# Kernel tuning notes

Measured on AMD Instinct MI355X. Metric: run time of the kernel, lower is better.

The kernel has to match this reference:

```python
import jax, jax.numpy as jnp
import numpy as np

# dims
N, T = 16, 2000            # batch, encoder frames
ENC, DEC = 512, 512        # enc_dim, dec_dim
ATT, C, K, H = 512, 10, 64, 4  # att_dim, conv_channels, loc_context, att_head


def setup_inputs() -> dict:
    key = jax.random.key(0)
    ks = jax.random.split(key, 16)
    s = 0.02
    enc_pad = jax.random.normal(ks[0], (N, T, ENC), jnp.float32)
    enc_len = jax.random.randint(ks[1], (N,), T // 2, T + 1, jnp.int32)
    dec_prev = jax.random.normal(ks[2], (N, DEC), jnp.float32)
    ali_prev = jax.random.uniform(ks[3], (N, H, T), jnp.float32)
    ali_prev = ali_prev / ali_prev.sum(-1, keepdims=True)
    # parameters (torch layout)
    We = jax.random.normal(ks[4], (ATT * H, ENC), jnp.float32) * s   # enc_proj weight
    be = jnp.zeros((ATT * H,), jnp.float32)                          # enc_proj bias
    Wk = jax.random.normal(ks[5], (ATT * H, ENC), jnp.float32) * s   # key_proj
    Wd = jax.random.normal(ks[6], (ATT * H, DEC), jnp.float32) * s   # dec_proj
    WF = jax.random.normal(ks[7], (C * H, 1, 2 * K + 1), jnp.float32) * s  # F: grouped conv1d
    bF = jnp.zeros((C * H,), jnp.float32)
    Wa = jax.random.normal(ks[8], (H, ATT, C), jnp.float32) * s      # att: 1x1 grouped conv, per-head [ATT,C]
    Ww = jax.random.normal(ks[9], (H, ATT), jnp.float32) * s         # w: 1x1 grouped conv, per-head [ATT]
    Wc = jax.random.normal(ks[10], (ENC, ATT * H), jnp.float32) * s  # ctx_proj
    bc = jnp.zeros((ENC,), jnp.float32)
    return {"enc_pad": enc_pad, "enc_len": enc_len, "dec_prev": dec_prev,
            "ali_prev": ali_prev, "We": We, "be": be, "Wk": Wk, "Wd": Wd,
            "WF": WF, "bF": bF, "Wa": Wa, "Ww": Ww, "Wc": Wc, "bc": bc}


def reference(enc_pad, enc_len, dec_prev, ali_prev, We, be, Wk, Wd, WF, bF, Wa, Ww, Wc, bc):
    n, t, _ = enc_pad.shape
    # enc_part: N x H x T x D
    ep = enc_pad @ We.T + be
    enc_part = ep.reshape(n, t, H, ATT).transpose(0, 2, 1, 3)
    # key_part: N x H x D x T (matches torch transpose(1,2).view ordering)
    kp = enc_pad @ Wk.T
    key_part = kp.transpose(0, 2, 1).reshape(n, H, ATT, t)
    # pad mask: N x T, True where padded
    pad_mask = jnp.arange(t)[None, :] >= enc_len[:, None]
    # location features: grouped conv1d over alignment, per head
    f = jax.lax.conv_general_dilated(
        ali_prev, WF, window_strides=(1,), padding=[(K, K)],
        dimension_numbers=("NCH", "OIH", "NCH"), feature_group_count=H)
    f = (f + bF[None, :, None]).reshape(n, H, C, t)
    # 1x1 grouped conv: C -> ATT per head
    att_part = jnp.einsum("hdc,nhct->nhdt", Wa, f)
    dec_part = (dec_prev @ Wd.T).reshape(n, H, ATT)
    sum_part = jnp.tanh(att_part + key_part + dec_part[..., None])  # N x H x D x T
    score = jnp.einsum("hd,nhdt->nht", Ww, sum_part)                # N x H x T
    score = jnp.where(pad_mask[:, None, :], -jnp.inf, score)
    ali = jax.nn.softmax(score, axis=-1)
    ctx = jnp.einsum("nht,nhtd->nhd", ali, enc_part).reshape(n, H * ATT)
    ctx = ctx @ Wc.T + bc
    return ali, ctx
```

## Files before the change

kernel.cpp:

```cpp
#include <hip/hip_runtime.h>

#define NB   16
#define TT   2000
#define TP   2048
#define ENC  512
#define ATTD 512
#define HH   4
#define CC   10
#define KK   64
#define KW   129
#define HATT 2048

typedef unsigned short u16;
typedef __attribute__((ext_vector_type(8))) short bf16x8;
typedef __attribute__((ext_vector_type(4))) float f32x4;

#define AS1 __attribute__((address_space(1)))
#define AS3 __attribute__((address_space(3)))

__device__ inline unsigned bfpack2(float lo, float hi) {
    unsigned a = __builtin_bit_cast(unsigned, lo);
    unsigned b = __builtin_bit_cast(unsigned, hi);
    a = (a + 0x7fffu + ((a >> 16) & 1u)) >> 16;
    b = (b + 0x7fffu + ((b >> 16) & 1u)) >> 16;
    return a | (b << 16);
}

__global__ __launch_bounds__(256) void prep_kernel(
    const float* __restrict__ enc, const float* __restrict__ Wk,
    const float* __restrict__ ali_prev, const float* __restrict__ WF,
    const float* __restrict__ bF, const float* __restrict__ dec_prev,
    const float* __restrict__ Wd, const float* __restrict__ Wa,
    u16* __restrict__ Abf, u16* __restrict__ Wkbf,
    u16* __restrict__ ftb, u16* __restrict__ wab,
    float* __restrict__ decp)
{
    __shared__ union {
        struct { float aliW[632]; float wfT[KW * CC]; float bfs[CC]; } cv;
        float dsl[16 * 128];
    } sm;
    const int bid = blockIdx.x, tid = threadIdx.x;

    if (bid < 8704) {
        long long gid = ((long long)bid * 256 + tid) * 8;
        const long long ATOT = (long long)NB * TP * ENC;
        if (gid < ATOT) {
            int n = (int)(gid >> 20);
            int rem = (int)(gid & ((1 << 20) - 1));
            int r = rem >> 9, e = rem & 511;
            uint4 out;
            if (r < TT) {
                const float* s = enc + ((long long)n * TT + r) * ENC + e;
                float4 v0 = *(const float4*)s;
                float4 v1 = *(const float4*)(s + 4);
                out.x = bfpack2(v0.x, v0.y); out.y = bfpack2(v0.z, v0.w);
                out.z = bfpack2(v1.x, v1.y); out.w = bfpack2(v1.z, v1.w);
            } else {
                out.x = out.y = out.z = out.w = 0u;
            }
            *(uint4*)(Abf + gid) = out;
        } else {
            long long j = gid - ATOT;
            const float* s = Wk + j;
            float4 v0 = *(const float4*)s;
            float4 v1 = *(const float4*)(s + 4);
            uint4 out;
            out.x = bfpack2(v0.x, v0.y); out.y = bfpack2(v0.z, v0.w);
            out.z = bfpack2(v1.x, v1.y); out.w = bfpack2(v1.z, v1.w);
            *(uint4*)(Wkbf + j) = out;
        }
    } else if (bid < 8960) {
        int b2 = bid - 8704;
        int tc = b2 & 3, h = (b2 >> 2) & 3, n = b2 >> 4;
        int t0 = tc * 500;
        float* aliW = sm.cv.aliW;
        float* wfT  = sm.cv.wfT;
        float* bfs  = sm.cv.bfs;
        const float* arow = ali_prev + ((long long)n * HH + h) * TT;
        for (int i = tid; i < 632; i += 256) {
            int tt = t0 - KK + i;
            aliW[i] = (tt >= 0 && tt < TT) ? arow[tt] : 0.f;
        }
        for (int i = tid; i < KW * CC; i += 256) {
            int k = i / CC, c = i - k * CC;
            wfT[i] = WF[(h * CC + c) * KW + k];
        }
        if (tid < CC) bfs[tid] = bF[h * CC + tid];
        __syncthreads();
        if (tid < 250) {
            float acc0[CC], acc1[CC];
            #pragma unroll
            for (int c = 0; c < CC; c++) { acc0[c] = 0.f; acc1[c] = 0.f; }
            const int base = 2 * tid;
            float2 w0 = *(const float2*)&aliW[base];
            for (int k = 0; k < 128; k += 2) {
                float2 w2 = *(const float2*)&aliW[base + k + 2];
                #pragma unroll
                for (int cj = 0; cj < 5; cj++) {
                    float2 fk  = *(const float2*)&wfT[k * CC + cj * 2];
                    float2 fk1 = *(const float2*)&wfT[(k + 1) * CC + cj * 2];
                    acc0[2*cj]   += w0.x * fk.x + w0.y * fk1.x;
                    acc0[2*cj+1] += w0.x * fk.y + w0.y * fk1.y;
                    acc1[2*cj]   += w0.y * fk.x + w2.x * fk1.x;
                    acc1[2*cj+1] += w0.y * fk.y + w2.x * fk1.y;
                }
                w0 = w2;
            }
            #pragma unroll
            for (int cj = 0; cj < 5; cj++) {
                float2 fk = *(const float2*)&wfT[128 * CC + cj * 2];
                acc0[2*cj]   += w0.x * fk.x;  acc0[2*cj+1] += w0.x * fk.y;
                acc1[2*cj]   += w0.y * fk.x;  acc1[2*cj+1] += w0.y * fk.y;
            }
            #pragma unroll
            for (int c = 0; c < CC; c++) { acc0[c] += bfs[c]; acc1[c] += bfs[c]; }
            int t = t0 + base;
            u16* frow = ftb + (((long long)(n * HH + h)) * TP + t) * 16;
            uint4 ra, rb;
            ra.x = bfpack2(acc0[0], acc0[1]); ra.y = bfpack2(acc0[2], acc0[3]);
            ra.z = bfpack2(acc0[4], acc0[5]); ra.w = bfpack2(acc0[6], acc0[7]);
            rb.x = bfpack2(acc0[8], acc0[9]); rb.y = 0u; rb.z = 0u; rb.w = 0u;
            *(uint4*)(frow)     = ra; *(uint4*)(frow + 8)  = rb;
            ra.x = bfpack2(acc1[0], acc1[1]); ra.y = bfpack2(acc1[2], acc1[3]);
            ra.z = bfpack2(acc1[4], acc1[5]); ra.w = bfpack2(acc1[6], acc1[7]);
            rb.x = bfpack2(acc1[8], acc1[9]);
            *(uint4*)(frow + 16) = ra; *(uint4*)(frow + 24) = rb;
        } else if (tc == 3) {
            uint4 z = {0u, 0u, 0u, 0u};
            int r0 = 2000 + (tid - 250) * 8;
            u16* frow = ftb + (((long long)(n * HH + h)) * TP + r0) * 16;
            for (int r = 0; r < 8; r++) {
                *(uint4*)(frow + r * 16)     = z;
                *(uint4*)(frow + r * 16 + 8) = z;
            }
        }
    } else if (bid < 8992) {
        int b2 = bid - 8960;
        int kc = b2 >> 3, jc = b2 & 7;
        for (int i = tid; i < 2048; i += 256) {
            int nn = i >> 7, kk = i & 127;
            sm.dsl[i] = dec_prev[nn * 512 + kc * 128 + kk];
        }
        __syncthreads();
        int d = jc * 256 + tid;
        float acc[NB];
        #pragma unroll
        for (int n = 0; n < NB; n++) acc[n] = 0.f;
        const float4* w4 = (const float4*)(Wd + (long long)d * 512 + kc * 128);
        for (int e4 = 0; e4 < 32; e4++) {
            float4 w = w4[e4];
            #pragma unroll
            for (int n = 0; n < NB; n++) {
                const float* a = sm.dsl + n * 128 + e4 * 4;
                acc[n] += w.x * a[0] + w.y * a[1] + w.z * a[2] + w.w * a[3];
            }
        }
        #pragma unroll
        for (int n = 0; n < NB; n++) decp[((long long)kc * NB + n) * HATT + d] = acc[n];
    } else {
        int b2 = bid - 8992;
        int j0 = b2 * 512 + tid * 2;
        #pragma unroll
        for (int q = 0; q < 2; q++) {
            int j = j0 + q;
            int hh = j >> 9, dd = j & 511;
            const float* wr = Wa + ((long long)(hh * ATTD + dd)) * CC;
            uint4 ra, rb;
            ra.x = bfpack2(wr[0], wr[1]); ra.y = bfpack2(wr[2], wr[3]);
            ra.z = bfpack2(wr[4], wr[5]); ra.w = bfpack2(wr[6], wr[7]);
            rb.x = bfpack2(wr[8], wr[9]); rb.y = 0u; rb.z = 0u; rb.w = 0u;
            u16* out = wab + (long long)j * 16;
            *(uint4*)(out)     = ra;
            *(uint4*)(out + 8) = rb;
        }
    }
}

__global__ __launch_bounds__(256, 4) void score_gemm_kernel(
    const u16* __restrict__ Abf, const u16* __restrict__ Bbf,
    const u16* __restrict__ ftb, const u16* __restrict__ wab,
    const float* __restrict__ decp, const float* __restrict__ Ww,
    const int* __restrict__ enc_len, float* __restrict__ score_part)
{
    __shared__ __attribute__((aligned(16))) char smem[40960];
    float* sred = (float*)smem;

    const int bid = blockIdx.x;
    const int swz = (bid & 7) * 512 + (bid >> 3);
    const int nt = swz & 15, mt = (swz >> 4) & 15, n = swz >> 8;

    if (mt * 128 >= enc_len[n]) return;

    const int tid = threadIdx.x, wave = tid >> 6, lane = tid & 63;
    const int l16 = lane & 15, lk = lane >> 4;
    const int h = nt >> 2;

    const u16* Aptr = Abf + ((long long)n * TP + mt * 128) * ENC;
    const u16* Bptr = Bbf + (long long)nt * 128 * ENC;

    f32x4 acc[4][4];
    #pragma unroll
    for (int mi = 0; mi < 4; mi++)
        #pragma unroll
        for (int nj = 0; nj < 4; nj++) {
            f32x4 z = {0.f, 0.f, 0.f, 0.f};
            acc[mi][nj] = z;
        }

    const int wrow = (wave >> 1) * 64, wcol = (wave & 1) * 64;
    const int t0 = mt * 128, dd0 = (nt & 3) * 128;

    {
        const char* eAsrc = (const char*)(ftb + (((long long)(n * HH + h)) * TP + t0) * 16);
        const char* eBsrc = (const char*)(wab + (long long)nt * 128 * 16);
        __builtin_amdgcn_global_load_lds(
            (const AS1 void*)(eAsrc + tid * 16),
            (AS3 void*)(smem + 32768 + wave * 1024), 16, 0, 0);
        __builtin_amdgcn_global_load_lds(
            (const AS1 void*)(eBsrc + tid * 16),
            (AS3 void*)(smem + 36864 + wave * 1024), 16, 0, 0);
    }

    for (int kt = 0; kt < 8; kt++) {
        const int k0 = kt * 64;
        #pragma unroll
        for (int i = 0; i < 4; i++) {
            int b = i * 4096 + tid * 16;
            int r = b >> 7, kb = b & 127;
            int kbs = kb ^ ((r & 7) << 4);
            __builtin_amdgcn_global_load_lds(
                (const AS1 void*)(Aptr + r * ENC + k0 + (kbs >> 1)),
                (AS3 void*)(smem + i * 4096 + wave * 1024), 16, 0, 0);
            __builtin_amdgcn_global_load_lds(
                (const AS1 void*)(Bptr + r * ENC + k0 + (kbs >> 1)),
                (AS3 void*)(smem + 16384 + i * 4096 + wave * 1024), 16, 0, 0);
        }
        __syncthreads();
        #pragma unroll
        for (int ks = 0; ks < 64; ks += 32) {
            bf16x8 af[4], bf[4];
            #pragma unroll
            for (int mi = 0; mi < 4; mi++) {
                int row = wrow + mi * 16 + l16;
                int cb = (ks * 2 + lk * 16) ^ ((row & 7) << 4);
                af[mi] = *(const bf16x8*)(smem + row * 128 + cb);
            }
            #pragma unroll
            for (int nj = 0; nj < 4; nj++) {
                int row = wcol + nj * 16 + l16;
                int cb = (ks * 2 + lk * 16) ^ ((row & 7) << 4);
                bf[nj] = *(const bf16x8*)(smem + 16384 + row * 128 + cb);
            }
            #pragma unroll
            for (int mi = 0; mi < 4; mi++)
                #pragma unroll
                for (int nj = 0; nj < 4; nj++)
                    acc[mi][nj] = __builtin_amdgcn_mfma_f32_16x16x32_bf16(
                        af[mi], bf[nj], acc[mi][nj], 0, 0, 0);
        }
        __syncthreads();
    }

    {
        const u16* eA = (const u16*)(smem + 32768);
        const u16* eB = (const u16*)(smem + 36864);
        bf16x8 zer = {0, 0, 0, 0, 0, 0, 0, 0};
        bf16x8 af[4], bf[4];
        #pragma unroll
        for (int mi = 0; mi < 4; mi++) {
            af[mi] = zer;
            if (lk < 2) af[mi] = *(const bf16x8*)(eA + (wrow + mi * 16 + l16) * 16 + lk * 8);
        }
        #pragma unroll
        for (int nj = 0; nj < 4; nj++) {
            bf[nj] = zer;
            if (lk < 2) bf[nj] = *(const bf16x8*)(eB + (wcol + nj * 16 + l16) * 16 + lk * 8);
        }
        #pragma unroll
        for (int mi = 0; mi < 4; mi++)
            #pragma unroll
            for (int nj = 0; nj < 4; nj++)
                acc[mi][nj] = __builtin_amdgcn_mfma_f32_16x16x32_bf16(
                    af[mi], bf[nj], acc[mi][nj], 0, 0, 0);
    }

    float wm2[4], dec4[4];
    #pragma unroll
    for (int nj = 0; nj < 4; nj++) {
        int cl = wcol + nj * 16 + l16;
        wm2[nj] = -2.f * Ww[h * ATTD + dd0 + cl];
        int j = nt * 128 + cl;
        dec4[nj] = decp[((long long)0 * NB + n) * HATT + j]
                 + decp[((long long)1 * NB + n) * HATT + j]
                 + decp[((long long)2 * NB + n) * HATT + j]
                 + decp[((long long)3 * NB + n) * HATT + j];
    }

    #pragma unroll
    for (int mi = 0; mi < 4; mi++) {
        #pragma unroll
        for (int j = 0; j < 4; j++) {
            int rl = wrow + mi * 16 + lk * 4 + j;
            float s = 0.f;
            #pragma unroll
            for (int nj = 0; nj < 4; nj++) {
                float v = acc[mi][nj][j] + dec4[nj];
                float e = __expf(v + v);
                s = fmaf(wm2[nj], __builtin_amdgcn_rcpf(e + 1.f), s);
            }
            s += __shfl_xor(s, 1); s += __shfl_xor(s, 2);
            s += __shfl_xor(s, 4); s += __shfl_xor(s, 8);
            if (l16 == 0) sred[(wave & 1) * 128 + rl] = s;
        }
    }
    __syncthreads();
    if (tid < 128) {
        int t = t0 + tid;
        if (t < TT)
            score_part[((long long)((nt & 3) * NB + n) * HH + h) * TT + t] =
                sred[tid] + sred[128 + tid];
    }
}

__global__ __launch_bounds__(256) void softmax_kernel(
    const float* __restrict__ score_part, const int* __restrict__ enc_len,
    float* __restrict__ ali)
{
    int n = blockIdx.x >> 2, h = blockIdx.x & 3;
    int len = enc_len[n];
    int tid = threadIdx.x;
    float s[8];
    float lmax = -3.4e38f;
    #pragma unroll
    for (int i = 0; i < 8; i++) {
        int t = tid + i * 256;
        float v = -3.4e38f;
        if (t < len) {
            v = 0.f;
            #pragma unroll
            for (int q = 0; q < 4; q++)
                v += score_part[((long long)(q * NB + n) * HH + h) * TT + t];
        }
        s[i] = v;
        lmax = fmaxf(lmax, v);
    }
    __shared__ float red[256];
    red[tid] = lmax; __syncthreads();
    for (int off = 128; off; off >>= 1) {
        if (tid < off) red[tid] = fmaxf(red[tid], red[tid + off]);
        __syncthreads();
    }
    float bmax = red[0];
    __syncthreads();
    float lsum = 0.f;
    #pragma unroll
    for (int i = 0; i < 8; i++) {
        int t = tid + i * 256;
        if (t < len) { s[i] = expf(s[i] - bmax); lsum += s[i]; }
        else s[i] = 0.f;
    }
    red[tid] = lsum; __syncthreads();
    for (int off = 128; off; off >>= 1) {
        if (tid < off) red[tid] += red[tid + off];
        __syncthreads();
    }
    float inv = 1.f / red[0];
    float* arow = ali + ((long long)n * HH + h) * TT;
    #pragma unroll
    for (int i = 0; i < 8; i++) {
        int t = tid + i * 256;
        if (t < TT) arow[t] = s[i] * inv;
    }
}

__global__ __launch_bounds__(256) void a_enc_kernel(
    const float* __restrict__ ali, const u16* __restrict__ Abf,
    const int* __restrict__ enc_len, float* __restrict__ a_enc_part)
{
    int tc = blockIdx.x & 31, n = blockIdx.x >> 5;
    int tid = threadIdx.x;
    int len = enc_len[n];
    int tbeg = tc * 63;
    int cnt = len - tbeg; if (cnt > 63) cnt = 63; if (cnt < 0) cnt = 0;
    __shared__ float aliS[HH][64];
    {
        int hh = tid >> 6, tt = tid & 63;
        aliS[hh][tt] = (tt < cnt) ? ali[((long long)n * HH + hh) * TT + tbeg + tt] : 0.f;
    }
    __syncthreads();
    float acc[HH][2];
    #pragma unroll
    for (int hh = 0; hh < HH; hh++) { acc[hh][0] = 0.f; acc[hh][1] = 0.f; }
    #pragma unroll 4
    for (int tt = 0; tt < cnt; tt++) {
        int t = tbeg + tt;
        float w0 = aliS[0][tt], w1 = aliS[1][tt], w2 = aliS[2][tt], w3 = aliS[3][tt];
        unsigned u = *(const unsigned*)(Abf + ((long long)n * TP + t) * ENC + tid * 2);
        float ex = __builtin_bit_cast(float, u << 16);
        float ey = __builtin_bit_cast(float, u & 0xffff0000u);
        acc[0][0] += w0 * ex; acc[0][1] += w0 * ey;
        acc[1][0] += w1 * ex; acc[1][1] += w1 * ey;
        acc[2][0] += w2 * ex; acc[2][1] += w2 * ey;
        acc[3][0] += w3 * ex; acc[3][1] += w3 * ey;
    }
    #pragma unroll
    for (int hh = 0; hh < HH; hh++) {
        a_enc_part[(((long long)tc * NB + n) * HH + hh) * ENC + tid * 2 + 0] = acc[hh][0];
        a_enc_part[(((long long)tc * NB + n) * HH + hh) * ENC + tid * 2 + 1] = acc[hh][1];
    }
}

__global__ __launch_bounds__(256) void ctx_tmp_kernel(
    const float* __restrict__ a_enc_part, const float* __restrict__ We,
    const float* __restrict__ be, float* __restrict__ ctmp)
{
    int kc = blockIdx.x >> 3, jc = blockIdx.x & 7;
    int tid = threadIdx.x;
    int j = jc * 256 + tid;
    int h = j >> 9;
    __shared__ float aes[16 * 128];
    for (int i = tid; i < 2048; i += 256) {
        int nn = i >> 7, kk = i & 127;
        float s = 0.f;
        for (int tc = 0; tc < 32; tc++)
            s += a_enc_part[(((long long)tc * NB + nn) * HH + h) * ENC + kc * 128 + kk];
        aes[i] = s;
    }
    __syncthreads();
    float acc[NB];
    #pragma unroll
    for (int n = 0; n < NB; n++) acc[n] = 0.f;
    const float4* w4 = (const float4*)(We + (long long)j * 512 + kc * 128);
    for (int e4 = 0; e4 < 32; e4++) {
        float4 w = w4[e4];
        #pragma unroll
        for (int n = 0; n < NB; n++) {
            const float* a = aes + n * 128 + e4 * 4;
            acc[n] += w.x * a[0] + w.y * a[1] + w.z * a[2] + w.w * a[3];
        }
    }
    float bias = (kc == 0) ? be[j] : 0.f;
    #pragma unroll
    for (int n = 0; n < NB; n++)
        ctmp[((long long)kc * NB + n) * HATT + j] = acc[n] + bias;
}

__global__ __launch_bounds__(256) void ctx_out_kernel(
    const float* __restrict__ ctmp, const float* __restrict__ Wc,
    const float* __restrict__ bc, float* __restrict__ out_ctx)
{
    int ec = blockIdx.x & 7, nc = blockIdx.x >> 3;
    int tid = threadIdx.x;
    __shared__ float ct[8 * 2048];
    __shared__ float red[4][64][8];
    for (int i = tid; i < 8 * 2048; i += 256) {
        int nn = i >> 11, j = i & 2047;
        int n = nc * 8 + nn;
        ct[i] = ctmp[((long long)0 * NB + n) * HATT + j]
              + ctmp[((long long)1 * NB + n) * HATT + j]
              + ctmp[((long long)2 * NB + n) * HATT + j]
              + ctmp[((long long)3 * NB + n) * HATT + j];
    }
    __syncthreads();
    int eo = tid & 63, kq = tid >> 6;
    int eg = ec * 64 + eo;
    float acc[8];
    #pragma unroll
    for (int nn = 0; nn < 8; nn++) acc[nn] = 0.f;
    const float4* w4 = (const float4*)(Wc + (long long)eg * HATT + kq * 512);
    for (int j4 = 0; j4 < 128; j4++) {
        float4 w = w4[j4];
        #pragma unroll
        for (int nn = 0; nn < 8; nn++) {
            const float* a = ct + nn * 2048 + kq * 512 + j4 * 4;
            acc[nn] += w.x * a[0] + w.y * a[1] + w.z * a[2] + w.w * a[3];
        }
    }
    #pragma unroll
    for (int nn = 0; nn < 8; nn++) red[kq][eo][nn] = acc[nn];
    __syncthreads();
    #pragma unroll
    for (int r = 0; r < 2; r++) {
        int idx = tid + r * 256;
        int eo2 = idx & 63, nn2 = idx >> 6;
        float s = red[0][eo2][nn2] + red[1][eo2][nn2]
                + red[2][eo2][nn2] + red[3][eo2][nn2];
        out_ctx[((long long)(nc * 8 + nn2)) * 512 + ec * 64 + eo2] = s + bc[ec * 64 + eo2];
    }
}

extern "C" void kernel_launch(void* const* d_in, const int* in_sizes, int n_in,
                              void* d_out, int out_size, void* d_ws, size_t ws_size,
                              hipStream_t stream)
{
    (void)in_sizes; (void)n_in; (void)out_size; (void)ws_size;
    const float* enc_pad  = (const float*)d_in[0];
    const int*   enc_len  = (const int*)  d_in[1];
    const float* dec_prev = (const float*)d_in[2];
    const float* ali_prev = (const float*)d_in[3];
    const float* We = (const float*)d_in[4];
    const float* be = (const float*)d_in[5];
    const float* Wk = (const float*)d_in[6];
    const float* Wd = (const float*)d_in[7];
    const float* WF = (const float*)d_in[8];
    const float* bF = (const float*)d_in[9];
    const float* Wa = (const float*)d_in[10];
    const float* Ww = (const float*)d_in[11];
    const float* Wc = (const float*)d_in[12];
    const float* bc = (const float*)d_in[13];

    char* ws = (char*)d_ws;
    u16*   Abf  = (u16*)  (ws);
    u16*   Wkbf = (u16*)  (ws + 33554432);
    u16*   ftb  = (u16*)  (ws + 35651584);
    u16*   wab  = (u16*)  (ws + 39845888);
    float* decp = (float*)(ws + 39911424);
    float* spart= (float*)(ws + 40435712);
    float* aep  = (float*)(ws + 40435712);
    float* ctmp = (float*)(ws + 39911424);

    float* ali = (float*)d_out;
    float* ctx = (float*)d_out + NB * HH * TT;

    prep_kernel      <<<8996, 256, 0, stream>>>(enc_pad, Wk, ali_prev, WF, bF,
                                                dec_prev, Wd, Wa,
                                                Abf, Wkbf, ftb, wab, decp);
    score_gemm_kernel<<<4096, 256, 0, stream>>>(Abf, Wkbf, ftb, wab, decp, Ww,
                                                enc_len, spart);
    softmax_kernel   <<<64,   256, 0, stream>>>(spart, enc_len, ali);
    a_enc_kernel     <<<512,  256, 0, stream>>>(ali, Abf, enc_len, aep);
    ctx_tmp_kernel   <<<32,   256, 0, stream>>>(aep, We, be, ctmp);
    ctx_out_kernel   <<<16,   256, 0, stream>>>(ctmp, Wc, bc, ctx);
}
```

Measured before the change: 191.8 us.

## Skip padded rows, vectorise softmax/a_enc, and widen ctx kernels' grids

The prep kernel now converts only encoder rows below each sequence's length and no longer writes zeros for padded rows. Score partials use a padded 2048 stride so the softmax can read and write them with float4. The a_enc kernel splits time across two thread halves, loads 4 bf16 per lane and reduces through shared memory. ctx_tmp and ctx_out double their block counts by halving their K/E chunks, and ctmp moves in the workspace to hold 8 partial slices. Skipping padded rows leaves stale data in Abf, so correctness depends on every consumer masking by enc_len; the score GEMM reads those rows too.

Measured after the change: 182.6 us. 1.05x faster.

```diff
diff --git a/kernel.cpp b/kernel.cpp
--- a/kernel.cpp
+++ b/kernel.cpp
@@ -3,6 +3,7 @@
 #define NB   16
 #define TT   2000
 #define TP   2048
+#define SPT  2048
 #define ENC  512
 #define ATTD 512
 #define HH   4
@@ -31,6 +32,7 @@
     const float* __restrict__ ali_prev, const float* __restrict__ WF,
     const float* __restrict__ bF, const float* __restrict__ dec_prev,
     const float* __restrict__ Wd, const float* __restrict__ Wa,
+    const int* __restrict__ enc_len,
     u16* __restrict__ Abf, u16* __restrict__ Wkbf,
     u16* __restrict__ ftb, u16* __restrict__ wab,
     float* __restrict__ decp)
@@ -48,17 +50,15 @@
             int n = (int)(gid >> 20);
             int rem = (int)(gid & ((1 << 20) - 1));
             int r = rem >> 9, e = rem & 511;
-            uint4 out;
-            if (r < TT) {
+            if (r < enc_len[n]) {
                 const float* s = enc + ((long long)n * TT + r) * ENC + e;
                 float4 v0 = *(const float4*)s;
                 float4 v1 = *(const float4*)(s + 4);
+                uint4 out;
                 out.x = bfpack2(v0.x, v0.y); out.y = bfpack2(v0.z, v0.w);
                 out.z = bfpack2(v1.x, v1.y); out.w = bfpack2(v1.z, v1.w);
-            } else {
-                out.x = out.y = out.z = out.w = 0u;
-            }
-            *(uint4*)(Abf + gid) = out;
+                *(uint4*)(Abf + gid) = out;
+            }
         } else {
             long long j = gid - ATOT;
             const float* s = Wk + j;
@@ -317,7 +317,7 @@
     if (tid < 128) {
         int t = t0 + tid;
         if (t < TT)
-            score_part[((long long)((nt & 3) * NB + n) * HH + h) * TT + t] =
+            score_part[((long long)((nt & 3) * NB + n) * HH + h) * SPT + t] =
                 sred[tid] + sred[128 + tid];
     }
 }
@@ -329,20 +329,22 @@
     int n = blockIdx.x >> 2, h = blockIdx.x & 3;
     int len = enc_len[n];
     int tid = threadIdx.x;
+    int t0 = tid * 8;
     float s[8];
+    #pragma unroll
+    for (int i = 0; i < 8; i++) s[i] = 0.f;
+    #pragma unroll
+    for (int q = 0; q < 4; q++) {
+        const float* rb = score_part + (((long long)(q * NB + n)) * HH + h) * SPT + t0;
+        float4 a = *(const float4*)rb;
+        float4 b = *(const float4*)(rb + 4);
+        s[0] += a.x; s[1] += a.y; s[2] += a.z; s[3] += a.w;
+        s[4] += b.x; s[5] += b.y; s[6] += b.z; s[7] += b.w;
+    }
     float lmax = -3.4e38f;
     #pragma unroll
     for (int i = 0; i < 8; i++) {
-        int t = tid + i * 256;
-        float v = -3.4e38f;
-        if (t < len) {
-            v = 0.f;
-            #pragma unroll
-            for (int q = 0; q < 4; q++)
-                v += score_part[((long long)(q * NB + n) * HH + h) * TT + t];
-        }
-        s[i] = v;
-        lmax = fmaxf(lmax, v);
+        if (t0 + i < len) lmax = fmaxf(lmax, s[i]);
     }
     __shared__ float red[256];
     red[tid] = lmax; __syncthreads();
@@ -355,8 +357,7 @@
     float lsum = 0.f;
     #pragma unroll
     for (int i = 0; i < 8; i++) {
-        int t = tid + i * 256;
-        if (t < len) { s[i] = expf(s[i] - bmax); lsum += s[i]; }
+        if (t0 + i < len) { s[i] = expf(s[i] - bmax); lsum += s[i]; }
         else s[i] = 0.f;
     }
     red[tid] = lsum; __syncthreads();
@@ -366,16 +367,20 @@
     }
     float inv = 1.f / red[0];
     float* arow = ali + ((long long)n * HH + h) * TT;
-    #pragma unroll
-    for (int i = 0; i < 8; i++) {
-        int t = tid + i * 256;
-        if (t < TT) arow[t] = s[i] * inv;
+    if (t0 + 8 <= TT) {
+        float4 o0 = {s[0] * inv, s[1] * inv, s[2] * inv, s[3] * inv};
+        float4 o1 = {s[4] * inv, s[5] * inv, s[6] * inv, s[7] * inv};
+        *(float4*)(arow + t0) = o0;
+        *(float4*)(arow + t0 + 4) = o1;
+    } else {
+        for (int i = 0; i < 8; i++)
+            if (t0 + i < TT) arow[t0 + i] = s[i] * inv;
     }
 }
 
 __global__ __launch_bounds__(256) void a_enc_kernel(
     const float* __restrict__ ali, const u16* __restrict__ Abf,
-    const int* __restrict__ enc_len, float* __restrict__ a_enc_part)
+    const int* __restrict__ enc_len, float* __restrict__ aep)
 {
     int tc = blockIdx.x & 31, n = blockIdx.x >> 5;
     int tid = threadIdx.x;
@@ -383,59 +388,75 @@
     int tbeg = tc * 63;
     int cnt = len - tbeg; if (cnt > 63) cnt = 63; if (cnt < 0) cnt = 0;
     __shared__ float aliS[HH][64];
+    __shared__ float red[2][4][129];
     {
         int hh = tid >> 6, tt = tid & 63;
         aliS[hh][tt] = (tt < cnt) ? ali[((long long)n * HH + hh) * TT + tbeg + tt] : 0.f;
     }
     __syncthreads();
-    float acc[HH][2];
-    #pragma unroll
-    for (int hh = 0; hh < HH; hh++) { acc[hh][0] = 0.f; acc[hh][1] = 0.f; }
-    #pragma unroll 4
-    for (int tt = 0; tt < cnt; tt++) {
-        int t = tbeg + tt;
-        float w0 = aliS[0][tt], w1 = aliS[1][tt], w2 = aliS[2][tt], w3 = aliS[3][tt];
-        unsigned u = *(const unsigned*)(Abf + ((long long)n * TP + t) * ENC + tid * 2);
-        float ex = __builtin_bit_cast(float, u << 16);
-        float ey = __builtin_bit_cast(float, u & 0xffff0000u);
-        acc[0][0] += w0 * ex; acc[0][1] += w0 * ey;
-        acc[1][0] += w1 * ex; acc[1][1] += w1 * ey;
-        acc[2][0] += w2 * ex; acc[2][1] += w2 * ey;
-        acc[3][0] += w3 * ex; acc[3][1] += w3 * ey;
+    const int l = tid & 127, tq = tid >> 7;
+    float acc[HH][4];
+    #pragma unroll
+    for (int hh = 0; hh < HH; hh++)
+        #pragma unroll
+        for (int k = 0; k < 4; k++) acc[hh][k] = 0.f;
+    for (int ii = 0; ii < 32; ii++) {
+        int tl = ii * 2 + tq;
+        if (tl < cnt) {
+            uint2 u = *(const uint2*)(Abf + ((long long)n * TP + tbeg + tl) * ENC + l * 4);
+            float e0 = __builtin_bit_cast(float, u.x << 16);
+            float e1 = __builtin_bit_cast(float, u.x & 0xffff0000u);
+            float e2 = __builtin_bit_cast(float, u.y << 16);
+            float e3 = __builtin_bit_cast(float, u.y & 0xffff0000u);
+            #pragma unroll
+            for (int hh = 0; hh < HH; hh++) {
+                float w = aliS[hh][tl];
+                acc[hh][0] += w * e0; acc[hh][1] += w * e1;
+                acc[hh][2] += w * e2; acc[hh][3] += w * e3;
+            }
+        }
     }
     #pragma unroll
     for (int hh = 0; hh < HH; hh++) {
-        a_enc_part[(((long long)tc * NB + n) * HH + hh) * ENC + tid * 2 + 0] = acc[hh][0];
-        a_enc_part[(((long long)tc * NB + n) * HH + hh) * ENC + tid * 2 + 1] = acc[hh][1];
+        __syncthreads();
+        #pragma unroll
+        for (int k = 0; k < 4; k++) red[tq][k][l] = acc[hh][k];
+        __syncthreads();
+        int d2 = tid * 2;
+        float v0 = red[0][d2 & 3][d2 >> 2] + red[1][d2 & 3][d2 >> 2];
+        int d3 = d2 + 1;
+        float v1 = red[0][d3 & 3][d3 >> 2] + red[1][d3 & 3][d3 >> 2];
+        float2 o = {v0, v1};
+        *(float2*)(aep + (((long long)tc * NB + n) * HH + hh) * ENC + d2) = o;
     }
 }
 
 __global__ __launch_bounds__(256) void ctx_tmp_kernel(
-    const float* __restrict__ a_enc_part, const float* __restrict__ We,
+    const float* __restrict__ aep, const float* __restrict__ We,
     const float* __restrict__ be, float* __restrict__ ctmp)
 {
     int kc = blockIdx.x >> 3, jc = blockIdx.x & 7;
     int tid = threadIdx.x;
     int j = jc * 256 + tid;
     int h = j >> 9;
-    __shared__ float aes[16 * 128];
-    for (int i = tid; i < 2048; i += 256) {
-        int nn = i >> 7, kk = i & 127;
+    __shared__ float aes[16 * 64];
+    for (int i = tid; i < 1024; i += 256) {
+        int nn = i >> 6, kk = i & 63;
         float s = 0.f;
         for (int tc = 0; tc < 32; tc++)
-            s += a_enc_part[(((long long)tc * NB + nn) * HH + h) * ENC + kc * 128 + kk];
+            s += aep[(((long long)tc * NB + nn) * HH + h) * ENC + kc * 64 + kk];
         aes[i] = s;
     }
     __syncthreads();
     float acc[NB];
     #pragma unroll
     for (int n = 0; n < NB; n++) acc[n] = 0.f;
-    const float4* w4 = (const float4*)(We + (long long)j * 512 + kc * 128);
-    for (int e4 = 0; e4 < 32; e4++) {
+    const float4* w4 = (const float4*)(We + (long long)j * 512 + kc * 64);
+    for (int e4 = 0; e4 < 16; e4++) {
         float4 w = w4[e4];
         #pragma unroll
         for (int n = 0; n < NB; n++) {
-            const float* a = aes + n * 128 + e4 * 4;
+            const float* a = aes + n * 64 + e4 * 4;
             acc[n] += w.x * a[0] + w.y * a[1] + w.z * a[2] + w.w * a[3];
         }
     }
@@ -449,43 +470,43 @@
     const float* __restrict__ ctmp, const float* __restrict__ Wc,
     const float* __restrict__ bc, float* __restrict__ out_ctx)
 {
-    int ec = blockIdx.x & 7, nc = blockIdx.x >> 3;
+    int ec = blockIdx.x & 15, nc = blockIdx.x >> 4;
     int tid = threadIdx.x;
     __shared__ float ct[8 * 2048];
-    __shared__ float red[4][64][8];
+    __shared__ float red[8][8][33];
     for (int i = tid; i < 8 * 2048; i += 256) {
         int nn = i >> 11, j = i & 2047;
         int n = nc * 8 + nn;
-        ct[i] = ctmp[((long long)0 * NB + n) * HATT + j]
-              + ctmp[((long long)1 * NB + n) * HATT + j]
-              + ctmp[((long long)2 * NB + n) * HATT + j]
-              + ctmp[((long long)3 * NB + n) * HATT + j];
+        float s = 0.f;
+        #pragma unroll
+        for (int kc = 0; kc < 8; kc++)
+            s += ctmp[((long long)kc * NB + n) * HATT + j];
+        ct[i] = s;
     }
     __syncthreads();
-    int eo = tid & 63, kq = tid >> 6;
-    int eg = ec * 64 + eo;
+    int eo = tid & 31, kq = tid >> 5;
+    int eg = ec * 32 + eo;
     float acc[8];
     #pragma unroll
     for (int nn = 0; nn < 8; nn++) acc[nn] = 0.f;
-    const float4* w4 = (const float4*)(Wc + (long long)eg * HATT + kq * 512);
-    for (int j4 = 0; j4 < 128; j4++) {
+    const float4* w4 = (const float4*)(Wc + (long long)eg * HATT + kq * 256);
+    for (int j4 = 0; j4 < 64; j4++) {
         float4 w = w4[j4];
         #pragma unroll
         for (int nn = 0; nn < 8; nn++) {
-            const float* a = ct + nn * 2048 + kq * 512 + j4 * 4;
+            const float* a = ct + nn * 2048 + kq * 256 + j4 * 4;
             acc[nn] += w.x * a[0] + w.y * a[1] + w.z * a[2] + w.w * a[3];
         }
     }
     #pragma unroll
-    for (int nn = 0; nn < 8; nn++) red[kq][eo][nn] = acc[nn];
+    for (int nn = 0; nn < 8; nn++) red[kq][nn][eo] = acc[nn];
     __syncthreads();
-    #pragma unroll
-    for (int r = 0; r < 2; r++) {
-        int idx = tid + r * 256;
-        int eo2 = idx & 63, nn2 = idx >> 6;
-        float s = red[0][eo2][nn2] + red[1][eo2][nn2]
-                + red[2][eo2][nn2] + red[3][eo2][nn2];
-        out_ctx[((long long)(nc * 8 + nn2)) * 512 + ec * 64 + eo2] = s + bc[ec * 64 + eo2];
+    {
+        int eo2 = tid & 31, nn2 = tid >> 5;
+        float s = 0.f;
+        #pragma unroll
+        for (int kq2 = 0; kq2 < 8; kq2++) s += red[kq2][nn2][eo2];
+        out_ctx[((long long)(nc * 8 + nn2)) * 512 + ec * 32 + eo2] = s + bc[ec * 32 + eo2];
     }
 }
 
@@ -517,18 +538,18 @@
     float* decp = (float*)(ws + 39911424);
     float* spart= (float*)(ws + 40435712);
     float* aep  = (float*)(ws + 40435712);
-    float* ctmp = (float*)(ws + 39911424);
+    float* ctmp = (float*)(ws + 35651584);
 
     float* ali = (float*)d_out;
     float* ctx = (float*)d_out + NB * HH * TT;
 
     prep_kernel      <<<8996, 256, 0, stream>>>(enc_pad, Wk, ali_prev, WF, bF,
-                                                dec_prev, Wd, Wa,
+                                                dec_prev, Wd, Wa, enc_len,
                                                 Abf, Wkbf, ftb, wab, decp);
     score_gemm_kernel<<<4096, 256, 0, stream>>>(Abf, Wkbf, ftb, wab, decp, Ww,
                                                 enc_len, spart);
     softmax_kernel   <<<64,   256, 0, stream>>>(spart, enc_len, ali);
     a_enc_kernel     <<<512,  256, 0, stream>>>(ali, Abf, enc_len, aep);
-    ctx_tmp_kernel   <<<32,   256, 0, stream>>>(aep, We, be, ctmp);
-    ctx_out_kernel   <<<16,   256, 0, stream>>>(ctmp, Wc, bc, ctx);
-}
+    ctx_tmp_kernel   <<<64,   256, 0, stream>>>(aep, We, be, ctmp);
+    ctx_out_kernel   <<<32,   256, 0, stream>>>(ctmp, Wc, bc, ctx);
+}
```
